# Optimization experiments

Hardware: AMD Instinct MI355X
Metric: run time of the kernel (lower is better)

The kernel has to match this reference:

```python
import jax, jax.numpy as jnp
import numpy as np

NHEADS = 16
NGROUPS = 16
NEG = -1e9

def _apply_rope(t, cos, sin):
    # t: (B,T,H,hs) -> pairs (B,T,H,hs//2,2); complex multiply by (cos + i*sin)
    B, T, H, hs = t.shape
    tp = t.reshape(B, T, H, hs // 2, 2)
    a, b = tp[..., 0], tp[..., 1]
    c = cos[None, :, None, :]
    s = sin[None, :, None, :]
    out = jnp.stack([a * c - b * s, a * s + b * c], axis=-1)
    return out.reshape(B, T, H, hs)

def _causal_attn(q, k, v):
    # q,k: (..., S, d); v: (..., S, dv); causal softmax attention, scale 1/sqrt(d)
    d = q.shape[-1]
    S = q.shape[-2]
    scores = jnp.einsum('...qd,...kd->...qk', q, k) / jnp.sqrt(jnp.asarray(d, q.dtype))
    mask = jnp.tril(jnp.ones((S, S), dtype=bool))
    scores = jnp.where(mask, scores, NEG)
    p = jax.nn.softmax(scores, axis=-1)
    return jnp.einsum('...qk,...kd->...qd', p, v)

def setup_inputs() -> dict:
    key = jax.random.key(0)
    k1, k2, k3 = jax.random.split(key, 3)
    B, T, C = 4, 2048, 1024
    hs = C // NHEADS
    x = jax.random.normal(k1, (B, T, C), dtype=jnp.float32)
    w_attn = jax.random.normal(k2, (3 * C, C), dtype=jnp.float32) * (1.0 / np.sqrt(C))
    w_proj = jax.random.normal(k3, (C, C), dtype=jnp.float32) * (1.0 / np.sqrt(C))
    # standard RoPE frequencies: theta_i = 10000^{-2i/hs}
    inv = 1.0 / (10000.0 ** (np.arange(0, hs, 2, dtype=np.float32) / hs))  # (hs//2,)
    ang = np.arange(T, dtype=np.float32)[:, None] * inv[None, :]           # (T, hs//2)
    freqs_cos = jnp.asarray(np.cos(ang), dtype=jnp.float32)
    freqs_sin = jnp.asarray(np.sin(ang), dtype=jnp.float32)
    return {'x': x, 'w_attn': w_attn, 'w_proj': w_proj,
            'freqs_cos': freqs_cos, 'freqs_sin': freqs_sin}

def reference(x, w_attn, w_proj, freqs_cos, freqs_sin):
    B, T, C = x.shape
    H = NHEADS
    hs = C // H
    G = min(T // (T // NGROUPS), NGROUPS)  # group_t = block_size // ngroups, T == block_size
    Tg = T // G
    qkv = x @ w_attn.T                      # (B,T,3C)
    q, k, v = jnp.split(qkv, 3, axis=2)
    # RoPE
    q = _apply_rope(q.reshape(B, T, H, hs), freqs_cos, freqs_sin).reshape(B, T, C)
    k = _apply_rope(k.reshape(B, T, H, hs), freqs_cos, freqs_sin).reshape(B, T, C)
    # group: (B, G, Tg, H, hs) -> (B, H, G, Tg, hs)
    def grp(t):
        return t.reshape(B, G, Tg, H, hs).transpose(0, 3, 1, 2, 4)
    q, k, v = grp(q), grp(k), grp(v)
    # its_time branch: append mean-pooled summary token per group
    q = jnp.concatenate([q, q.mean(axis=3, keepdims=True)], axis=3)  # (B,H,G,Tg+1,hs)
    k = jnp.concatenate([k, k.mean(axis=3, keepdims=True)], axis=3)
    v = jnp.concatenate([v, v.mean(axis=3, keepdims=True)], axis=3)
    att = _causal_attn(q, k, v)             # (B,H,G,Tg+1,hs)
    # group-level attention over summary tokens of all but last group
    q2 = q[:, :, :-1, -1]                   # (B,H,G-1,hs)
    k2 = k[:, :, :-1, -1]
    av = att[:, :, :-1, -1]                 # (B,H,G-1,hs)
    v2 = _causal_attn(q2, k2, av)           # (B,H,G-1,hs)
    y_q = q2[:, :, :, None, :]              # (B,H,G-1,1,hs)
    y_k = k2[:, :, :, None, :]
    y_v = v2[:, :, :, None, :]
    # drop summary tokens, merge groups back: (B,H,G,Tg,hs) -> (B,T,C)
    xo = att[:, :, :, :-1]
    xo = xo.reshape(B, H, T, hs).transpose(0, 2, 1, 3).reshape(B, T, C)
    out = xo @ w_proj.T
    return (out, y_q, y_k, y_v)
```

## Files before the change

### kernel.cpp

```cpp
#include <hip/hip_runtime.h>
#include <hip/hip_bf16.h>

#define HS 64
#define NH 16
#define NG 16
#define TT 2048
#define CC 1024
#define BBATCH 4
#define TG 128
#define SS 129

typedef __attribute__((ext_vector_type(8))) short bf16x8;
typedef __attribute__((ext_vector_type(4))) float f32x4;

__device__ __forceinline__ float bf2f(ushort u) {
  return __uint_as_float(((unsigned)u) << 16);
}
__device__ __forceinline__ ushort f2bf(float f) {
  unsigned x = __float_as_uint(f);
  x += 0x7fff + ((x >> 16) & 1);
  return (ushort)(x >> 16);
}
__device__ __forceinline__ bf16x8 mk8(ushort4 a0, ushort4 a1) {
  bf16x8 v;
  v[0] = (short)a0.x; v[1] = (short)a0.y; v[2] = (short)a0.z; v[3] = (short)a0.w;
  v[4] = (short)a1.x; v[5] = (short)a1.y; v[6] = (short)a1.z; v[7] = (short)a1.w;
  return v;
}

__global__ void cvt_f32_bf16(const float* __restrict__ src, ushort* __restrict__ dst, int n4) {
  int stride = gridDim.x * blockDim.x;
  for (int i = blockIdx.x * blockDim.x + threadIdx.x; i < n4; i += stride) {
    float4 v = ((const float4*)src)[i];
    ushort4 o;
    o.x = f2bf(v.x); o.y = f2bf(v.y); o.z = f2bf(v.z); o.w = f2bf(v.w);
    ((ushort4*)dst)[i] = o;
  }
}

template <bool OUT_BF16>
__global__ __launch_bounds__(256) void gemm_bt(const ushort* __restrict__ A,
                                               const ushort* __restrict__ Bw,
                                               void* __restrict__ Cout,
                                               int M, int N, int K) {
  __shared__ ushort As[128][68];
  __shared__ ushort Bs[128][68];
  const int m0 = blockIdx.y * 128;
  const int n0 = blockIdx.x * 128;
  const int tid = threadIdx.x;
  const int lane = tid & 63;
  const int wv = tid >> 6;
  const int wr = wv >> 1, wc = wv & 1;
  const int lo = lane & 15, hi = lane >> 4;

  f32x4 acc[4][4];
#pragma unroll
  for (int i = 0; i < 4; ++i)
#pragma unroll
    for (int j = 0; j < 4; ++j) acc[i][j] = (f32x4)0.0f;

  for (int k0 = 0; k0 < K; k0 += 64) {
    __syncthreads();
#pragma unroll
    for (int t = 0; t < 4; ++t) {
      int c = tid + 256 * t;
      int row = c >> 3, cc = c & 7;
      uint4 va = *(const uint4*)(A + (size_t)(m0 + row) * K + k0 + cc * 8);
      *(uint2*)&As[row][cc * 8]     = make_uint2(va.x, va.y);
      *(uint2*)&As[row][cc * 8 + 4] = make_uint2(va.z, va.w);
      uint4 vb = *(const uint4*)(Bw + (size_t)(n0 + row) * K + k0 + cc * 8);
      *(uint2*)&Bs[row][cc * 8]     = make_uint2(vb.x, vb.y);
      *(uint2*)&Bs[row][cc * 8 + 4] = make_uint2(vb.z, vb.w);
    }
    __syncthreads();
#pragma unroll
    for (int kk = 0; kk < 64; kk += 32) {
      bf16x8 af[4], bfr[4];
#pragma unroll
      for (int i = 0; i < 4; ++i) {
        int r = wr * 64 + i * 16 + lo;
        af[i] = mk8(*(const ushort4*)&As[r][kk + 4 * hi],
                    *(const ushort4*)&As[r][kk + 16 + 4 * hi]);
      }
#pragma unroll
      for (int j = 0; j < 4; ++j) {
        int r = wc * 64 + j * 16 + lo;
        bfr[j] = mk8(*(const ushort4*)&Bs[r][kk + 4 * hi],
                     *(const ushort4*)&Bs[r][kk + 16 + 4 * hi]);
      }
#pragma unroll
      for (int i = 0; i < 4; ++i)
#pragma unroll
        for (int j = 0; j < 4; ++j)
          acc[i][j] = __builtin_amdgcn_mfma_f32_16x16x32_bf16(af[i], bfr[j], acc[i][j], 0, 0, 0);
    }
  }
#pragma unroll
  for (int i = 0; i < 4; ++i) {
    int row = m0 + wr * 64 + i * 16 + 4 * hi;
#pragma unroll
    for (int j = 0; j < 4; ++j) {
      int col = n0 + wc * 64 + j * 16 + lo;
#pragma unroll
      for (int r = 0; r < 4; ++r) {
        float v = acc[i][j][r];
        if constexpr (OUT_BF16) {
          ((ushort*)Cout)[(size_t)(row + r) * N + col] = f2bf(v);
        } else {
          ((float*)Cout)[(size_t)(row + r) * N + col] = v;
        }
      }
    }
  }
}

__global__ __launch_bounds__(256) void rope_group(const ushort* __restrict__ qkv,
                                                  const float* __restrict__ fc,
                                                  const float* __restrict__ fs,
                                                  ushort* __restrict__ qg, ushort* __restrict__ kg,
                                                  ushort* __restrict__ vg,
                                                  float* __restrict__ yq, float* __restrict__ yk) {
  int blk = blockIdx.x;
  int g = blk & 15, h = (blk >> 4) & 15, b = blk >> 8;
  int tid = threadIdx.x;
  int d2 = tid & 31, s0 = tid >> 5;
  size_t gbase = (size_t)blk * SS * HS;
  float sq0 = 0, sq1 = 0, sk0 = 0, sk1 = 0, sv0 = 0, sv1 = 0;
#pragma unroll
  for (int it = 0; it < 16; ++it) {
    int s = s0 + 8 * it;
    int t = g * TG + s;
    size_t rowoff = ((size_t)(b * TT + t)) * (3 * CC) + h * HS + 2 * d2;
    float c = fc[t * 32 + d2], sn = fs[t * 32 + d2];
    ushort2 qu = *(const ushort2*)(qkv + rowoff);
    float qa = bf2f(qu.x), qb = bf2f(qu.y);
    float rq0 = qa * c - qb * sn, rq1 = qa * sn + qb * c;
    ushort2 ku = *(const ushort2*)(qkv + rowoff + CC);
    float ka = bf2f(ku.x), kb = bf2f(ku.y);
    float rk0 = ka * c - kb * sn, rk1 = ka * sn + kb * c;
    ushort2 vu = *(const ushort2*)(qkv + rowoff + 2 * CC);
    float v0 = bf2f(vu.x), v1 = bf2f(vu.y);
    *(ushort2*)(qg + gbase + s * HS + 2 * d2) = make_ushort2(f2bf(rq0), f2bf(rq1));
    *(ushort2*)(kg + gbase + s * HS + 2 * d2) = make_ushort2(f2bf(rk0), f2bf(rk1));
    *(ushort2*)(vg + gbase + s * HS + 2 * d2) = vu;
    sq0 += rq0; sq1 += rq1; sk0 += rk0; sk1 += rk1; sv0 += v0; sv1 += v1;
  }
  __shared__ float red[256][6];
  red[tid][0] = sq0; red[tid][1] = sq1; red[tid][2] = sk0;
  red[tid][3] = sk1; red[tid][4] = sv0; red[tid][5] = sv1;
  __syncthreads();
  if (tid < 32) {
    float m[6];
#pragma unroll
    for (int c = 0; c < 6; ++c) {
      float acc = 0;
#pragma unroll
      for (int r = 0; r < 8; ++r) acc += red[r * 32 + tid][c];
      m[c] = acc * (1.0f / 128.0f);
    }
    *(ushort2*)(qg + gbase + 128 * HS + 2 * tid) = make_ushort2(f2bf(m[0]), f2bf(m[1]));
    *(ushort2*)(kg + gbase + 128 * HS + 2 * tid) = make_ushort2(f2bf(m[2]), f2bf(m[3]));
    *(ushort2*)(vg + gbase + 128 * HS + 2 * tid) = make_ushort2(f2bf(m[4]), f2bf(m[5]));
    if (g < 15) {
      size_t yo = ((size_t)(b * 16 + h) * 15 + g) * 64 + 2 * tid;
      yq[yo] = m[0]; yq[yo + 1] = m[1];
      yk[yo] = m[2]; yk[yo + 1] = m[3];
    }
  }
}

__global__ __launch_bounds__(256) void attn1(const ushort* __restrict__ qg,
                                             const ushort* __restrict__ kg,
                                             const ushort* __restrict__ vg,
                                             ushort* __restrict__ xo, float* __restrict__ attm) {
  __shared__ ushort qs[144][68];
  __shared__ ushort ks[144][68];
  __shared__ ushort vt[64][148];
  __shared__ ushort obuf[4][16][68];
  const int blk = blockIdx.x;
  const int g = blk & 15, h = (blk >> 4) & 15, b = blk >> 8;
  const int tid = threadIdx.x;
  const int lane = tid & 63, wv = tid >> 6;
  const int lo = lane & 15, hi = lane >> 4;
  const size_t gbase = (size_t)blk * SS * HS;

  {
    ushort* vflat = &vt[0][0];
    for (int idx = tid; idx < 64 * 148 / 4; idx += 256)
      *(ushort4*)(vflat + idx * 4) = make_ushort4(0, 0, 0, 0);
  }
  __syncthreads();
  for (int idx = tid; idx < 144 * 16; idx += 256) {
    int s = idx >> 4, c = (idx & 15) * 4;
    if (s < SS) {
      *(ushort4*)&qs[s][c] = *(const ushort4*)(qg + gbase + s * HS + c);
      *(ushort4*)&ks[s][c] = *(const ushort4*)(kg + gbase + s * HS + c);
      ushort4 v4 = *(const ushort4*)(vg + gbase + s * HS + c);
      vt[c][s] = v4.x; vt[c + 1][s] = v4.y; vt[c + 2][s] = v4.z; vt[c + 3][s] = v4.w;
    } else {
      *(ushort4*)&qs[s][c] = make_ushort4(0, 0, 0, 0);
      *(ushort4*)&ks[s][c] = make_ushort4(0, 0, 0, 0);
    }
  }
  __syncthreads();

#pragma unroll
  for (int ti = 0; ti < 3; ++ti) {
    const int t = (ti == 0) ? (8 - wv)
                : (ti == 1) ? ((wv == 3) ? 4 : (wv + 1))
                            : ((wv == 3) ? 0 : -1);
    if (t < 0) continue;
    const int q0 = t * 16;

    bf16x8 bq[2];
#pragma unroll
    for (int k2 = 0; k2 < 2; ++k2)
      bq[k2] = mk8(*(const ushort4*)&qs[q0 + lo][k2 * 32 + 4 * hi],
                   *(const ushort4*)&qs[q0 + lo][k2 * 32 + 16 + 4 * hi]);

    f32x4 sc[9];
#pragma unroll
    for (int n = 0; n < 9; ++n) sc[n] = (f32x4)0.0f;
#pragma unroll
    for (int n = 0; n < 9; ++n) {
      if (n > t) continue;
#pragma unroll
      for (int k2 = 0; k2 < 2; ++k2) {
        bf16x8 ak = mk8(*(const ushort4*)&ks[n * 16 + lo][k2 * 32 + 4 * hi],
                        *(const ushort4*)&ks[n * 16 + lo][k2 * 32 + 16 + 4 * hi]);
        sc[n] = __builtin_amdgcn_mfma_f32_16x16x32_bf16(ak, bq[k2], sc[n], 0, 0, 0);
      }
    }

    const int qi = q0 + lo;
    float mx = -INFINITY;
#pragma unroll
    for (int n = 0; n < 9; ++n) {
      if (n > t) continue;
#pragma unroll
      for (int r = 0; r < 4; ++r) {
        int kj = n * 16 + 4 * hi + r;
        float v = (kj <= qi) ? sc[n][r] * 0.125f : -INFINITY;
        sc[n][r] = v;
        mx = fmaxf(mx, v);
      }
    }
    mx = fmaxf(mx, __shfl_xor(mx, 16));
    mx = fmaxf(mx, __shfl_xor(mx, 32));
    float sum = 0.f;
#pragma unroll
    for (int n = 0; n < 9; ++n) {
      if (n > t) continue;
#pragma unroll
      for (int r = 0; r < 4; ++r) {
        float e = __expf(sc[n][r] - mx);
        sc[n][r] = e;
        sum += e;
      }
    }
    sum += __shfl_xor(sum, 16);
    sum += __shfl_xor(sum, 32);
    const float inv = 1.0f / sum;

    f32x4 oac[4];
#pragma unroll
    for (int m = 0; m < 4; ++m) oac[m] = (f32x4)0.0f;
#pragma unroll
    for (int s2 = 0; s2 < 5; ++s2) {
      if (s2 > (t >> 1)) continue;
      const int kt1ok = (2 * s2 + 1 <= t);
      bf16x8 pb;
#pragma unroll
      for (int e = 0; e < 4; ++e) pb[e] = (short)f2bf(sc[2 * s2][e] * inv);
      if (kt1ok) {
#pragma unroll
        for (int e = 0; e < 4; ++e) pb[e + 4] = (short)f2bf(sc[2 * s2 + 1][e] * inv);
      } else {
#pragma unroll
        for (int e = 0; e < 4; ++e) pb[e + 4] = 0;
      }
#pragma unroll
      for (int m = 0; m < 4; ++m) {
        ushort4 a0 = *(const ushort4*)&vt[m * 16 + lo][32 * s2 + 4 * hi];
        ushort4 a1 = kt1ok ? *(const ushort4*)&vt[m * 16 + lo][32 * s2 + 16 + 4 * hi]
                           : make_ushort4(0, 0, 0, 0);
        oac[m] = __builtin_amdgcn_mfma_f32_16x16x32_bf16(mk8(a0, a1), pb, oac[m], 0, 0, 0);
      }
    }

    if (t < 8) {
#pragma unroll
      for (int m = 0; m < 4; ++m)
#pragma unroll
        for (int r = 0; r < 4; ++r)
          obuf[wv][lo][m * 16 + 4 * hi + r] = f2bf(oac[m][r]);
#pragma unroll
      for (int it = 0; it < 4; ++it) {
        int idx = lane + 64 * it;
        int r = idx >> 4;
        int c4 = (idx & 15) * 4;
        uint2 val = *(const uint2*)&obuf[wv][r][c4];
        int tok = g * TG + t * 16 + r;
        *(uint2*)(xo + ((size_t)(b * TT + tok)) * CC + h * HS + c4) = val;
      }
    } else {
      if (lo == 0) {
#pragma unroll
        for (int m = 0; m < 4; ++m)
#pragma unroll
          for (int r = 0; r < 4; ++r)
            attm[(size_t)blk * 64 + m * 16 + 4 * hi + r] = oac[m][r];
      }
    }
  }
}

__global__ __launch_bounds__(64) void attn2(const float* __restrict__ yq,
                                            const float* __restrict__ yk,
                                            const float* __restrict__ attm,
                                            float* __restrict__ yv) {
  __shared__ float qs2[15][64], ks2[15][64], avs[15][64], srow[16];
  int bh = blockIdx.x, lane = threadIdx.x;
  for (int j = 0; j < 15; ++j) {
    qs2[j][lane] = yq[((size_t)bh * 15 + j) * 64 + lane];
    ks2[j][lane] = yk[((size_t)bh * 15 + j) * 64 + lane];
    avs[j][lane] = attm[((size_t)bh * 16 + j) * 64 + lane];
  }
  __syncthreads();
  for (int i = 0; i < 15; ++i) {
    float qv = qs2[i][lane];
    for (int j = 0; j <= i; ++j) {
      float t = qv * ks2[j][lane];
#pragma unroll
      for (int off = 32; off > 0; off >>= 1) t += __shfl_xor(t, off);
      if (lane == 0) srow[j] = t * 0.125f;
    }
    __syncthreads();
    float mx = -INFINITY;
    for (int j = 0; j <= i; ++j) mx = fmaxf(mx, srow[j]);
    float den = 0;
    for (int j = 0; j <= i; ++j) den += __expf(srow[j] - mx);
    float inv = 1.0f / den;
    float o = 0;
    for (int j = 0; j <= i; ++j) o += __expf(srow[j] - mx) * inv * avs[j][lane];
    yv[((size_t)bh * 15 + i) * 64 + lane] = o;
    __syncthreads();
  }
}

extern "C" void kernel_launch(void* const* d_in, const int* in_sizes, int n_in,
                              void* d_out, int out_size, void* d_ws, size_t ws_size,
                              hipStream_t stream) {
  const float* x      = (const float*)d_in[0];
  const float* w_attn = (const float*)d_in[1];
  const float* w_proj = (const float*)d_in[2];
  const float* fc     = (const float*)d_in[3];
  const float* fs     = (const float*)d_in[4];
  float* out = (float*)d_out;

  char* ws = (char*)d_ws;
  ushort* xb   = (ushort*)(ws);
  ushort* xo   = (ushort*)(ws);
  ushort* wab  = (ushort*)(ws + 16777216);
  float*  attm = (float*) (ws + 16777216);
  ushort* wpb  = (ushort*)(ws + 23068672);
  ushort* qkv  = (ushort*)(ws + 25165824);
  ushort* qg   = (ushort*)(ws + 75497472);
  ushort* kg   = (ushort*)(ws + 92405760);
  ushort* vg   = (ushort*)(ws + 109314048);

  float* yq = out + 8388608;
  float* yk = out + 8450048;
  float* yv = out + 8511488;

  cvt_f32_bf16<<<2048, 256, 0, stream>>>(x, xb, 8388608 / 4);
  cvt_f32_bf16<<<1024, 256, 0, stream>>>(w_attn, wab, 3145728 / 4);
  cvt_f32_bf16<<<512, 256, 0, stream>>>(w_proj, wpb, 1048576 / 4);
  gemm_bt<true><<<dim3(24, 64), 256, 0, stream>>>(xb, wab, qkv, 8192, 3072, 1024);
  rope_group<<<1024, 256, 0, stream>>>(qkv, fc, fs, qg, kg, vg, yq, yk);
  attn1<<<1024, 256, 0, stream>>>(qg, kg, vg, xo, attm);
  attn2<<<64, 64, 0, stream>>>(yq, yk, attm, yv);
  gemm_bt<false><<<dim3(8, 64), 256, 0, stream>>>(xo, wpb, out, 8192, 1024, 1024);
}
```

Baseline: 199.4 us.

## Fuse RoPE and group pooling into attention kernel, merge conversion launches

```diff
diff --git a/kernel.cpp b/kernel.cpp
--- a/kernel.cpp
+++ b/kernel.cpp
@@ -28,13 +28,19 @@
   return v;
 }
 
-__global__ void cvt_f32_bf16(const float* __restrict__ src, ushort* __restrict__ dst, int n4) {
-  int stride = gridDim.x * blockDim.x;
-  for (int i = blockIdx.x * blockDim.x + threadIdx.x; i < n4; i += stride) {
-    float4 v = ((const float4*)src)[i];
+__global__ void cvt3(const float* __restrict__ x, const float* __restrict__ wa,
+                     const float* __restrict__ wp, ushort* __restrict__ xb,
+                     ushort* __restrict__ wab, ushort* __restrict__ wpb) {
+  const int stride = gridDim.x * blockDim.x;
+  for (int i = blockIdx.x * blockDim.x + threadIdx.x; i < 3145728; i += stride) {
+    const float* src; ushort* dst; int off;
+    if (i < 2097152) { src = x; dst = xb; off = i; }
+    else if (i < 2883584) { src = wa; dst = wab; off = i - 2097152; }
+    else { src = wp; dst = wpb; off = i - 2883584; }
+    float4 v = ((const float4*)src)[off];
     ushort4 o;
     o.x = f2bf(v.x); o.y = f2bf(v.y); o.z = f2bf(v.z); o.w = f2bf(v.w);
-    ((ushort4*)dst)[i] = o;
+    ((ushort4*)dst)[off] = o;
   }
 }
 
@@ -114,92 +120,83 @@
   }
 }
 
-__global__ __launch_bounds__(256) void rope_group(const ushort* __restrict__ qkv,
-                                                  const float* __restrict__ fc,
-                                                  const float* __restrict__ fs,
-                                                  ushort* __restrict__ qg, ushort* __restrict__ kg,
-                                                  ushort* __restrict__ vg,
-                                                  float* __restrict__ yq, float* __restrict__ yk) {
-  int blk = blockIdx.x;
-  int g = blk & 15, h = (blk >> 4) & 15, b = blk >> 8;
-  int tid = threadIdx.x;
-  int d2 = tid & 31, s0 = tid >> 5;
-  size_t gbase = (size_t)blk * SS * HS;
-  float sq0 = 0, sq1 = 0, sk0 = 0, sk1 = 0, sv0 = 0, sv1 = 0;
-#pragma unroll
-  for (int it = 0; it < 16; ++it) {
-    int s = s0 + 8 * it;
-    int t = g * TG + s;
-    size_t rowoff = ((size_t)(b * TT + t)) * (3 * CC) + h * HS + 2 * d2;
-    float c = fc[t * 32 + d2], sn = fs[t * 32 + d2];
-    ushort2 qu = *(const ushort2*)(qkv + rowoff);
-    float qa = bf2f(qu.x), qb = bf2f(qu.y);
-    float rq0 = qa * c - qb * sn, rq1 = qa * sn + qb * c;
-    ushort2 ku = *(const ushort2*)(qkv + rowoff + CC);
-    float ka = bf2f(ku.x), kb = bf2f(ku.y);
-    float rk0 = ka * c - kb * sn, rk1 = ka * sn + kb * c;
-    ushort2 vu = *(const ushort2*)(qkv + rowoff + 2 * CC);
-    float v0 = bf2f(vu.x), v1 = bf2f(vu.y);
-    *(ushort2*)(qg + gbase + s * HS + 2 * d2) = make_ushort2(f2bf(rq0), f2bf(rq1));
-    *(ushort2*)(kg + gbase + s * HS + 2 * d2) = make_ushort2(f2bf(rk0), f2bf(rk1));
-    *(ushort2*)(vg + gbase + s * HS + 2 * d2) = vu;
-    sq0 += rq0; sq1 += rq1; sk0 += rk0; sk1 += rk1; sv0 += v0; sv1 += v1;
-  }
-  __shared__ float red[256][6];
-  red[tid][0] = sq0; red[tid][1] = sq1; red[tid][2] = sk0;
-  red[tid][3] = sk1; red[tid][4] = sv0; red[tid][5] = sv1;
-  __syncthreads();
-  if (tid < 32) {
-    float m[6];
-#pragma unroll
-    for (int c = 0; c < 6; ++c) {
-      float acc = 0;
-#pragma unroll
-      for (int r = 0; r < 8; ++r) acc += red[r * 32 + tid][c];
-      m[c] = acc * (1.0f / 128.0f);
-    }
-    *(ushort2*)(qg + gbase + 128 * HS + 2 * tid) = make_ushort2(f2bf(m[0]), f2bf(m[1]));
-    *(ushort2*)(kg + gbase + 128 * HS + 2 * tid) = make_ushort2(f2bf(m[2]), f2bf(m[3]));
-    *(ushort2*)(vg + gbase + 128 * HS + 2 * tid) = make_ushort2(f2bf(m[4]), f2bf(m[5]));
-    if (g < 15) {
-      size_t yo = ((size_t)(b * 16 + h) * 15 + g) * 64 + 2 * tid;
-      yq[yo] = m[0]; yq[yo + 1] = m[1];
-      yk[yo] = m[2]; yk[yo + 1] = m[3];
-    }
-  }
-}
-
-__global__ __launch_bounds__(256) void attn1(const ushort* __restrict__ qg,
-                                             const ushort* __restrict__ kg,
-                                             const ushort* __restrict__ vg,
-                                             ushort* __restrict__ xo, float* __restrict__ attm) {
+__global__ __launch_bounds__(256) void attn1f(const ushort* __restrict__ qkv,
+                                              const float* __restrict__ fc,
+                                              const float* __restrict__ fs,
+                                              ushort* __restrict__ xo, float* __restrict__ attm,
+                                              float* __restrict__ yq, float* __restrict__ yk) {
   __shared__ ushort qs[144][68];
   __shared__ ushort ks[144][68];
   __shared__ ushort vt[64][148];
   __shared__ ushort obuf[4][16][68];
+  __shared__ float red[256][6];
   const int blk = blockIdx.x;
   const int g = blk & 15, h = (blk >> 4) & 15, b = blk >> 8;
   const int tid = threadIdx.x;
   const int lane = tid & 63, wv = tid >> 6;
   const int lo = lane & 15, hi = lane >> 4;
-  const size_t gbase = (size_t)blk * SS * HS;
+
+  for (int idx = tid; idx < 320; idx += 256) {
+    int d = idx / 5, ch = (idx % 5) * 4;
+    *(ushort4*)&vt[d][128 + ch] = make_ushort4(0, 0, 0, 0);
+  }
+  const size_t rowbase = (size_t)(b * TT + g * TG) * (3 * CC) + h * HS;
+  for (int idx = tid; idx < 3072; idx += 256) {
+    int part = idx >> 10, rem = idx & 1023, s = rem >> 3, c8 = (rem & 7) * 8;
+    uint4 w = *(const uint4*)(qkv + rowbase + (size_t)s * (3 * CC) + part * CC + c8);
+    if (part == 0) {
+      *(uint4*)&qs[s][c8] = w;
+    } else if (part == 1) {
+      *(uint4*)&ks[s][c8] = w;
+    } else {
+      ushort e[8];
+      *(uint4*)e = w;
+#pragma unroll
+      for (int j = 0; j < 8; ++j) vt[c8 + j][s] = e[j];
+    }
+  }
+  __syncthreads();
 
   {
-    ushort* vflat = &vt[0][0];
-    for (int idx = tid; idx < 64 * 148 / 4; idx += 256)
-      *(ushort4*)(vflat + idx * 4) = make_ushort4(0, 0, 0, 0);
+    const int d2 = tid & 31, sg = tid >> 5;
+    float sq0 = 0, sq1 = 0, sk0 = 0, sk1 = 0, sv0 = 0, sv1 = 0;
+#pragma unroll
+    for (int it = 0; it < 16; ++it) {
+      int s = sg + 8 * it;
+      int ts = g * TG + s;
+      float c = fc[ts * 32 + d2], sn = fs[ts * 32 + d2];
+      ushort2 qu = *(const ushort2*)&qs[s][2 * d2];
+      float qa = bf2f(qu.x), qb = bf2f(qu.y);
+      float rq0 = qa * c - qb * sn, rq1 = qa * sn + qb * c;
+      *(ushort2*)&qs[s][2 * d2] = make_ushort2(f2bf(rq0), f2bf(rq1));
+      ushort2 ku = *(const ushort2*)&ks[s][2 * d2];
+      float ka = bf2f(ku.x), kb = bf2f(ku.y);
+      float rk0 = ka * c - kb * sn, rk1 = ka * sn + kb * c;
+      *(ushort2*)&ks[s][2 * d2] = make_ushort2(f2bf(rk0), f2bf(rk1));
+      float v0 = bf2f(vt[2 * d2][s]), v1 = bf2f(vt[2 * d2 + 1][s]);
+      sq0 += rq0; sq1 += rq1; sk0 += rk0; sk1 += rk1; sv0 += v0; sv1 += v1;
+    }
+    red[tid][0] = sq0; red[tid][1] = sq1; red[tid][2] = sk0;
+    red[tid][3] = sk1; red[tid][4] = sv0; red[tid][5] = sv1;
   }
   __syncthreads();
-  for (int idx = tid; idx < 144 * 16; idx += 256) {
-    int s = idx >> 4, c = (idx & 15) * 4;
-    if (s < SS) {
-      *(ushort4*)&qs[s][c] = *(const ushort4*)(qg + gbase + s * HS + c);
-      *(ushort4*)&ks[s][c] = *(const ushort4*)(kg + gbase + s * HS + c);
-      ushort4 v4 = *(const ushort4*)(vg + gbase + s * HS + c);
-      vt[c][s] = v4.x; vt[c + 1][s] = v4.y; vt[c + 2][s] = v4.z; vt[c + 3][s] = v4.w;
-    } else {
-      *(ushort4*)&qs[s][c] = make_ushort4(0, 0, 0, 0);
-      *(ushort4*)&ks[s][c] = make_ushort4(0, 0, 0, 0);
+  if (tid < 32) {
+    float m[6];
+#pragma unroll
+    for (int c = 0; c < 6; ++c) {
+      float acc = 0;
+#pragma unroll
+      for (int r = 0; r < 8; ++r) acc += red[r * 32 + tid][c];
+      m[c] = acc * (1.0f / 128.0f);
+    }
+    *(ushort2*)&qs[128][2 * tid] = make_ushort2(f2bf(m[0]), f2bf(m[1]));
+    *(ushort2*)&ks[128][2 * tid] = make_ushort2(f2bf(m[2]), f2bf(m[3]));
+    vt[2 * tid][128] = f2bf(m[4]);
+    vt[2 * tid + 1][128] = f2bf(m[5]);
+    if (g < 15) {
+      size_t yo = ((size_t)(b * 16 + h) * 15 + g) * 64 + 2 * tid;
+      yq[yo] = m[0]; yq[yo + 1] = m[1];
+      yk[yo] = m[2]; yk[yo + 1] = m[3];
     }
   }
   __syncthreads();
@@ -365,20 +362,14 @@
   float*  attm = (float*) (ws + 16777216);
   ushort* wpb  = (ushort*)(ws + 23068672);
   ushort* qkv  = (ushort*)(ws + 25165824);
-  ushort* qg   = (ushort*)(ws + 75497472);
-  ushort* kg   = (ushort*)(ws + 92405760);
-  ushort* vg   = (ushort*)(ws + 109314048);
 
   float* yq = out + 8388608;
   float* yk = out + 8450048;
   float* yv = out + 8511488;
 
-  cvt_f32_bf16<<<2048, 256, 0, stream>>>(x, xb, 8388608 / 4);
-  cvt_f32_bf16<<<1024, 256, 0, stream>>>(w_attn, wab, 3145728 / 4);
-  cvt_f32_bf16<<<512, 256, 0, stream>>>(w_proj, wpb, 1048576 / 4);
+  cvt3<<<2048, 256, 0, stream>>>(x, w_attn, w_proj, xb, wab, wpb);
   gemm_bt<true><<<dim3(24, 64), 256, 0, stream>>>(xb, wab, qkv, 8192, 3072, 1024);
-  rope_group<<<1024, 256, 0, stream>>>(qkv, fc, fs, qg, kg, vg, yq, yk);
-  attn1<<<1024, 256, 0, stream>>>(qg, kg, vg, xo, attm);
+  attn1f<<<1024, 256, 0, stream>>>(qkv, fc, fs, xo, attm, yq, yk);
   attn2<<<64, 64, 0, stream>>>(yq, yk, attm, yv);
   gemm_bt<false><<<dim3(8, 64), 256, 0, stream>>>(xo, wpb, out, 8192, 1024, 1024);
 }
```

Measured after the change: 186.5 us. 6.5% less time.
